# Performance work log

Hardware: AMD Instinct MI355X
Metric: run time of the kernel (lower is better)

The kernel has to match this reference:

```python
import jax, jax.numpy as jnp
import numpy as np
import math

N = 512      # sequence length (residues)
CS = 384     # single_embedding_size
CZ = 128     # pair_embedding_size
C = 16       # ipa_embedding_size
PQ = 4       # num_query_points
PV = 8       # num_value_points
H = 12       # num_heads

SCALE_SINGLE = 1.0 / math.sqrt(C)
SCALE_FRAME = -1.0 / math.sqrt(18 * PQ)


def setup_inputs() -> dict:
    key = jax.random.key(0)
    ks = jax.random.split(key, 14)
    w = lambda k, shape: jax.random.normal(k, shape, dtype=jnp.float32) * 0.02
    return {
        "single_rep": jax.random.normal(ks[0], (N, CS), dtype=jnp.float32),
        "pair_rep": jax.random.normal(ks[1], (N, N, CZ), dtype=jnp.float32),
        "rotations": jax.random.normal(ks[2], (N, 3, 3), dtype=jnp.float32),
        "translations": jax.random.normal(ks[3], (N, 3), dtype=jnp.float32),
        "Wq": w(ks[4], (CS, H * C)),
        "Wk": w(ks[5], (CS, H * C)),
        "Wv": w(ks[6], (CS, H * C)),
        "Wqp": w(ks[7], (CS, H * PQ * 3)),
        "Wkp": w(ks[8], (CS, H * PQ * 3)),
        "Wvp": w(ks[9], (CS, H * PV * 3)),
        "Wb": w(ks[10], (CZ, H)),
        "Wout": w(ks[11], (H * (CZ + C + PV * 4), CS)),
        "bout": jnp.zeros((CS,), dtype=jnp.float32),
        "scale_head": jnp.ones((H,), dtype=jnp.float32),
    }


def reference(single_rep, pair_rep, rotations, translations,
              Wq, Wk, Wv, Wqp, Wkp, Wvp, Wb, Wout, bout, scale_head):
    n = single_rep.shape[0]

    def apply_frames(x):  # x: [n, h, p, 3] -> R_n x + t_n
        return jnp.einsum('nij,nhpj->nhpi', rotations, x) + translations[:, None, None, :]

    # projections
    q = (single_rep @ Wq).reshape(n, H, C)
    k = (single_rep @ Wk).reshape(n, H, C)
    v = (single_rep @ Wv).reshape(n, H, C)
    qp = (single_rep @ Wqp).reshape(n, H, PQ, 3)
    kp = (single_rep @ Wkp).reshape(n, H, PQ, 3)
    vp = (single_rep @ Wvp).reshape(n, H, PV, 3)

    # single-rep weight: [n, H, n]
    w_single = SCALE_SINGLE * jnp.einsum('nhc,mhc->nhm', q, k)

    # pair-rep bias weight: [n, H, n]
    w_pair = jnp.einsum('nmz,zh->nhm', pair_rep, Wb)

    # frame (point) weight
    lq = apply_frames(qp)  # [n,H,PQ,3]
    lk = apply_frames(kp)  # [n,H,PQ,3]
    diff = lq[:, None] - lk[None, :]                 # [n,n,H,PQ,3]
    d2 = jnp.sum(diff * diff, axis=(-1, -2))         # [n,n,H]
    w_frame = SCALE_FRAME * jax.nn.softplus(scale_head)[None, :, None] \
              * jnp.transpose(d2, (0, 2, 1))         # [n,H,n]

    weight = jax.nn.softmax(w_single + w_pair + w_frame, axis=-1)  # [n,H,n]

    # attentions
    o_single = jnp.einsum('nhm,mhc->nhc', weight, v)            # [n,H,C]
    o_pair = jnp.einsum('nhm,nmz->nhz', weight, pair_rep)       # [n,H,CZ]

    lvp = apply_frames(vp)                                      # [n,H,PV,3]
    o_local = jnp.einsum('nhm,mhpc->nhpc', weight, lvp)         # [n,H,PV,3]
    # inverse frame: R^T (x - t)
    o_frame = jnp.einsum('nji,nhpj->nhpi', rotations,
                         o_local - translations[:, None, None, :])  # [n,H,PV,3]
    o_norm = jnp.linalg.norm(o_frame, axis=-1)                  # [n,H,PV]

    att = jnp.concatenate(
        [o_single, o_pair, o_frame.reshape(n, H, PV * 3), o_norm], axis=-1)
    return att.reshape(n, -1) @ Wout + bout
```

## Files before the change

kernel.cpp:

```cpp
#include <hip/hip_runtime.h>
#include <math.h>

#define NRES 512
#define CSZ  384
#define CZ   128
#define CC   16
#define PQ   4
#define PV   8
#define NH   12

#define HC    (NH*CC)
#define HPQ3  (NH*PQ*3)
#define HPV3  (NH*PV*3)
#define ATTD  (NH*(CZ+CC+PV*4))

#define OFF_Q   0
#define OFF_K   (OFF_Q  + NRES*HC)
#define OFF_V   (OFF_K  + NRES*HC)
#define OFF_LQ  (OFF_V  + NRES*HC)
#define OFF_LK  (OFF_LQ + NRES*HPQ3)
#define OFF_LVP (OFF_LK + NRES*HPQ3)
#define OFF_ATT (OFF_LVP+ NRES*HPV3)
#define OFF_LOG (OFF_ATT + NRES*ATTD)
#define OFF_PART OFF_LOG
#define LOG_FLOATS (NRES*NH*NRES)

#define OFF_KH  OFF_ATT
#define OFF_QH  (OFF_ATT + NH*NRES*32)

#define SCALE_SINGLE 0.25f
#define SCALE_FRAME  (-0.1178511301977579f)

#define LROW 516

#define PJ_BM 32
#define PJ_BN 64
#define PJ_BK 32
#define PJ_NK (CSZ/PJ_BK)
#define PJ_AP 388

__global__ __launch_bounds__(256) void k_proj2(
    const float* __restrict__ S,
    const float* __restrict__ Wq, const float* __restrict__ Wk,
    const float* __restrict__ Wv, const float* __restrict__ Wqp,
    const float* __restrict__ Wkp, const float* __restrict__ Wvp,
    float* __restrict__ ws)
{
  __shared__ __align__(16) float A_s[PJ_BM][PJ_AP];
  __shared__ __align__(16) float B_s[PJ_BK][PJ_BN];

  const int t  = threadIdx.x;
  const int rb = blockIdx.x / 18;
  const int cb = blockIdx.x % 18;
  const int tc = t & 15, tr = t >> 4;

  #pragma unroll
  for (int j = 0; j < 12; ++j) {
    int idx = t + j*256;
    int row = idx / 96, kq = idx % 96;
    float4 v4 = *(const float4*)(S + (size_t)(rb*PJ_BM + row)*CSZ + kq*4);
    *(float4*)&A_s[row][kq*4] = v4;
  }

  const float* Wp[2]; int ncB[2], lcB[2], kkB[2], cqB[2];
  #pragma unroll
  for (int j = 0; j < 2; ++j) {
    int idx = t + j*256;
    int kk = idx >> 4, cq = idx & 15;
    kkB[j] = kk; cqB[j] = cq;
    int col = cb*PJ_BN + cq*4;
    if      (col < 192) { Wp[j]=Wq;  ncB[j]=192; lcB[j]=col;     }
    else if (col < 384) { Wp[j]=Wk;  ncB[j]=192; lcB[j]=col-192; }
    else if (col < 576) { Wp[j]=Wv;  ncB[j]=192; lcB[j]=col-384; }
    else if (col < 720) { Wp[j]=Wqp; ncB[j]=144; lcB[j]=col-576; }
    else if (col < 864) { Wp[j]=Wkp; ncB[j]=144; lcB[j]=col-720; }
    else                { Wp[j]=Wvp; ncB[j]=288; lcB[j]=col-864; }
  }

  float4 bw[2];
  #pragma unroll
  for (int j = 0; j < 2; ++j)
    bw[j] = *(const float4*)(Wp[j] + (size_t)kkB[j]*ncB[j] + lcB[j]);

  float acc[2][4];
  #pragma unroll
  for (int i=0;i<2;i++)
    #pragma unroll
    for (int jj=0;jj<4;jj++) acc[i][jj]=0.f;

  for (int ki = 0; ki < PJ_NK; ++ki) {
    __syncthreads();
    #pragma unroll
    for (int j = 0; j < 2; ++j)
      *(float4*)&B_s[kkB[j]][cqB[j]*4] = bw[j];
    __syncthreads();

    if (ki + 1 < PJ_NK) {
      #pragma unroll
      for (int j = 0; j < 2; ++j)
        bw[j] = *(const float4*)(Wp[j] + (size_t)((ki+1)*PJ_BK + kkB[j])*ncB[j] + lcB[j]);
    }

    #pragma unroll
    for (int kk4 = 0; kk4 < PJ_BK/4; ++kk4) {
      float4 a0 = *(const float4*)&A_s[tr*2+0][ki*PJ_BK + kk4*4];
      float4 a1 = *(const float4*)&A_s[tr*2+1][ki*PJ_BK + kk4*4];
      const float* a0p = (const float*)&a0;
      const float* a1p = (const float*)&a1;
      #pragma unroll
      for (int e = 0; e < 4; ++e) {
        float4 b4 = *(const float4*)&B_s[kk4*4+e][tc*4];
        float f0 = a0p[e], f1 = a1p[e];
        acc[0][0] += f0*b4.x; acc[0][1] += f0*b4.y; acc[0][2] += f0*b4.z; acc[0][3] += f0*b4.w;
        acc[1][0] += f1*b4.x; acc[1][1] += f1*b4.y; acc[1][2] += f1*b4.z; acc[1][3] += f1*b4.w;
      }
    }
  }

  {
    int col = cb*PJ_BN + tc*4;
    float* dst; int stride; int lcc;
    if      (col < 192) { dst = ws+OFF_Q;   stride=192; lcc=col;     }
    else if (col < 384) { dst = ws+OFF_K;   stride=192; lcc=col-192; }
    else if (col < 576) { dst = ws+OFF_V;   stride=192; lcc=col-384; }
    else if (col < 720) { dst = ws+OFF_LQ;  stride=144; lcc=col-576; }
    else if (col < 864) { dst = ws+OFF_LK;  stride=144; lcc=col-720; }
    else                { dst = ws+OFF_LVP; stride=288; lcc=col-864; }
    #pragma unroll
    for (int i = 0; i < 2; ++i) {
      int row = rb*PJ_BM + tr*2 + i;
      *(float4*)&dst[(size_t)row*stride + lcc] =
          make_float4(acc[i][0], acc[i][1], acc[i][2], acc[i][3]);
    }
  }
}

__global__ __launch_bounds__(256) void k_frames(
    const float* __restrict__ rot, const float* __restrict__ trans,
    float* __restrict__ ws)
{
  int gid = blockIdx.x*256 + threadIdx.x;
  if (gid >= NRES*192) return;
  int m = gid / 192;
  int rest = gid % 192;
  float* base; int pidx;
  if      (rest <  48) { base = ws + OFF_LQ  + (size_t)m*HPQ3; pidx = rest;     }
  else if (rest <  96) { base = ws + OFF_LK  + (size_t)m*HPQ3; pidx = rest-48;  }
  else                 { base = ws + OFF_LVP + (size_t)m*HPV3; pidx = rest-96;  }
  float x = base[pidx*3+0], y = base[pidx*3+1], z = base[pidx*3+2];
  const float* R = rot + (size_t)m*9;
  const float* T = trans + (size_t)m*3;
  float o0 = R[0]*x + R[1]*y + R[2]*z + T[0];
  float o1 = R[3]*x + R[4]*y + R[5]*z + T[1];
  float o2 = R[6]*x + R[7]*y + R[8]*z + T[2];
  base[pidx*3+0]=o0; base[pidx*3+1]=o1; base[pidx*3+2]=o2;
}

__global__ __launch_bounds__(256) void k_hat(
    const float* __restrict__ scale_head, float* __restrict__ ws)
{
  const int r = blockIdx.x;
  const int t = threadIdx.x;
  __shared__ float sSp[NH];
  if (t < NH) { float x = scale_head[t];
                sSp[t] = (x > 20.f) ? x : log1pf(__expf(x)); }
  __syncthreads();

  for (int i = t; i < NH*32; i += 256) {
    const int h = i >> 5, j = i & 31;
    const float* kk = ws + OFF_K  + (size_t)r*HC   + h*CC;
    const float* lk = ws + OFF_LK + (size_t)r*HPQ3 + h*12;
    const float* qq = ws + OFF_Q  + (size_t)r*HC   + h*CC;
    const float* lq = ws + OFF_LQ + (size_t)r*HPQ3 + h*12;
    float kv, qv;
    if (j < 16)      { kv = kk[j];    qv = SCALE_SINGLE * qq[j]; }
    else if (j < 28) { kv = lk[j-16]; qv = -2.f*SCALE_FRAME*sSp[h]*lq[j-16]; }
    else if (j == 28) {
      float s2 = 0.f;
      #pragma unroll
      for (int e=0;e<12;e++) { float v = lk[e]; s2 += v*v; }
      kv = SCALE_FRAME * sSp[h] * s2;
      qv = 1.f;
    } else { kv = 0.f; qv = 0.f; }
    ws[OFF_KH + ((size_t)h*NRES + r)*32 + j] = kv;
    ws[OFF_QH + ((size_t)h*NRES + r)*32 + j] = qv;
  }
}

#define QK_P 68
__global__ __launch_bounds__(256) void k_qk(float* __restrict__ ws)
{
  __shared__ __align__(16) float Qs[32*QK_P];
  __shared__ __align__(16) float Ks[32*QK_P];

  const int bid = blockIdx.x;
  const int h  = bid >> 6;
  const int nt = (bid >> 3) & 7;
  const int mt = bid & 7;
  const int t  = threadIdx.x;
  const int tc = t & 15, tr = t >> 4;

  const float4* qsrc = (const float4*)(ws + OFF_QH + ((size_t)h*NRES + nt*64)*32);
  const float4* ksrc = (const float4*)(ws + OFF_KH + ((size_t)h*NRES + mt*64)*32);

  #pragma unroll
  for (int u = 0; u < 2; ++u) {
    int idx = t + u*256;
    int r = idx >> 3, j4 = idx & 7;
    float4 qv = qsrc[idx];
    float4 kv = ksrc[idx];
    Qs[(j4*4+0)*QK_P + r] = qv.x;
    Qs[(j4*4+1)*QK_P + r] = qv.y;
    Qs[(j4*4+2)*QK_P + r] = qv.z;
    Qs[(j4*4+3)*QK_P + r] = qv.w;
    Ks[(j4*4+0)*QK_P + r] = kv.x;
    Ks[(j4*4+1)*QK_P + r] = kv.y;
    Ks[(j4*4+2)*QK_P + r] = kv.z;
    Ks[(j4*4+3)*QK_P + r] = kv.w;
  }
  __syncthreads();

  float acc[4][4];
  #pragma unroll
  for (int i=0;i<4;i++)
    #pragma unroll
    for (int k2=0;k2<4;k2++) acc[i][k2]=0.f;

  #pragma unroll
  for (int j = 0; j < 32; ++j) {
    float4 qv = *(const float4*)&Qs[j*QK_P + tr*4];
    float4 kv = *(const float4*)&Ks[j*QK_P + tc*4];
    acc[0][0] += qv.x*kv.x; acc[0][1] += qv.x*kv.y; acc[0][2] += qv.x*kv.z; acc[0][3] += qv.x*kv.w;
    acc[1][0] += qv.y*kv.x; acc[1][1] += qv.y*kv.y; acc[1][2] += qv.y*kv.z; acc[1][3] += qv.y*kv.w;
    acc[2][0] += qv.z*kv.x; acc[2][1] += qv.z*kv.y; acc[2][2] += qv.z*kv.z; acc[2][3] += qv.z*kv.w;
    acc[3][0] += qv.w*kv.x; acc[3][1] += qv.w*kv.y; acc[3][2] += qv.w*kv.z; acc[3][3] += qv.w*kv.w;
  }

  float* wlog = ws + OFF_LOG;
  #pragma unroll
  for (int i = 0; i < 4; ++i) {
    int n = nt*64 + tr*4 + i;
    *(float4*)&wlog[((size_t)n*NH + h)*NRES + mt*64 + tc*4] =
        make_float4(acc[i][0], acc[i][1], acc[i][2], acc[i][3]);
  }
}

__global__ __launch_bounds__(512) void k_attn2(
    const float* __restrict__ pair,
    const float* __restrict__ rot, const float* __restrict__ trans,
    const float* __restrict__ Wb,
    float* __restrict__ ws)
{
  const int n = blockIdx.x;
  const int t = threadIdx.x;

  __shared__ __align__(16) float sLogit[NH*LROW];
  __shared__ __align__(16) float sOP[4][NH*CZ];
  __shared__ __align__(16) float sOL[HPV3];
  __shared__ float sR[9];
  __shared__ float sT[3];

  const float* v    = ws + OFF_V;
  const float* lvp  = ws + OFF_LVP;
  const float* wlog = ws + OFF_LOG;
  float* att = ws + OFF_ATT;

  if (t >= 488 && t < 497)      sR[t-488] = rot[(size_t)n*9 + (t-488)];
  else if (t >= 497 && t < 500) sT[t-497] = trans[(size_t)n*3 + (t-497)];
  __syncthreads();

  {
    const int m = t;
    float acch[NH];
    #pragma unroll
    for (int h=0;h<NH;h++) acch[h]=0.f;

    const float4* pr = (const float4*)(pair + ((size_t)n*NRES + m)*CZ);
    for (int zq = 0; zq < CZ/4; ++zq) {
      float4 p4 = pr[zq];
      const float* pp = (const float*)&p4;
      #pragma unroll
      for (int e=0;e<4;e++) {
        float pv_ = pp[e];
        const float* wrow = Wb + (size_t)(zq*4+e)*NH;
        #pragma unroll
        for (int h=0;h<NH;h++) acch[h] += pv_ * wrow[h];
      }
    }

    #pragma unroll
    for (int h=0;h<NH;h++) {
      acch[h] += wlog[((size_t)n*NH + h)*NRES + m];
      sLogit[h*LROW + m] = acch[h];
    }
  }
  __syncthreads();

  {
    int wave = t >> 6, lane = t & 63;
    for (int h = wave; h < NH; h += 8) {
      float x[8]; float mx = -1e30f;
      #pragma unroll
      for (int j=0;j<8;j++) { x[j] = sLogit[h*LROW + lane + j*64]; mx = fmaxf(mx, x[j]); }
      #pragma unroll
      for (int d=1; d<64; d<<=1) mx = fmaxf(mx, __shfl_xor(mx, d, 64));
      float s = 0.f;
      #pragma unroll
      for (int j=0;j<8;j++) { x[j] = __expf(x[j]-mx); s += x[j]; }
      #pragma unroll
      for (int d=1; d<64; d<<=1) s += __shfl_xor(s, d, 64);
      float inv = 1.f/s;
      #pragma unroll
      for (int j=0;j<8;j++) sLogit[h*LROW + lane + j*64] = x[j]*inv;
    }
  }
  __syncthreads();

  {
    const int zq = t & 31;
    const int hg = (t >> 5) & 3;
    const int mg = t >> 7;
    float a0[4] = {0,0,0,0}, a1[4] = {0,0,0,0}, a2[4] = {0,0,0,0};
    const float* pb = pair + (size_t)n*NRES*CZ + zq*4;
    for (int mb = 0; mb < 32; ++mb) {
      int m0 = mg*128 + mb*4;
      float4 w0 = *(const float4*)&sLogit[(hg+0)*LROW + m0];
      float4 w1 = *(const float4*)&sLogit[(hg+4)*LROW + m0];
      float4 w2 = *(const float4*)&sLogit[(hg+8)*LROW + m0];
      const float* w0p = (const float*)&w0;
      const float* w1p = (const float*)&w1;
      const float* w2p = (const float*)&w2;
      #pragma unroll
      for (int i=0;i<4;i++) {
        float4 p4 = *(const float4*)(pb + (size_t)(m0+i)*CZ);
        const float* pp = (const float*)&p4;
        float f0 = w0p[i], f1 = w1p[i], f2 = w2p[i];
        #pragma unroll
        for (int e=0;e<4;e++) {
          a0[e] += f0*pp[e]; a1[e] += f1*pp[e]; a2[e] += f2*pp[e];
        }
      }
    }
    *(float4*)&sOP[mg][(hg+0)*CZ + zq*4] = make_float4(a0[0],a0[1],a0[2],a0[3]);
    *(float4*)&sOP[mg][(hg+4)*CZ + zq*4] = make_float4(a1[0],a1[1],a1[2],a1[3]);
    *(float4*)&sOP[mg][(hg+8)*CZ + zq*4] = make_float4(a2[0],a2[1],a2[2],a2[3]);
  }

  {
    if (t < 480) {
      float acc = 0.f;
      const float* src; int stride; int off; int h;
      if (t < 192) { h = t >> 4;        src = v;   stride = HC;   off = t;      }
      else         { int idx = t - 192; h = idx/24; src = lvp; stride = HPV3; off = idx; }
      const float* wrow = sLogit + h*LROW;
      for (int m0 = 0; m0 < NRES; m0 += 4) {
        float4 w4 = *(const float4*)&wrow[m0];
        acc += w4.x * src[(size_t)(m0+0)*stride + off];
        acc += w4.y * src[(size_t)(m0+1)*stride + off];
        acc += w4.z * src[(size_t)(m0+2)*stride + off];
        acc += w4.w * src[(size_t)(m0+3)*stride + off];
      }
      if (t < 192) {
        int h2 = t >> 4;
        att[(size_t)n*ATTD + h2*176 + (t & 15)] = acc;
      } else {
        sOL[t-192] = acc;
      }
    }
  }
  __syncthreads();

  for (int o = t; o < NH*CZ; o += 512) {
    float sres = sOP[0][o] + sOP[1][o] + sOP[2][o] + sOP[3][o];
    int h = o >> 7, z = o & 127;
    att[(size_t)n*ATTD + h*176 + 16 + z] = sres;
  }

  if (t < 96) {
    int h = t / 8, p = t % 8;
    float x = sOL[h*24 + p*3 + 0] - sT[0];
    float y = sOL[h*24 + p*3 + 1] - sT[1];
    float z = sOL[h*24 + p*3 + 2] - sT[2];
    float o0 = sR[0]*x + sR[3]*y + sR[6]*z;
    float o1 = sR[1]*x + sR[4]*y + sR[7]*z;
    float o2 = sR[2]*x + sR[5]*y + sR[8]*z;
    float nm = sqrtf(o0*o0 + o1*o1 + o2*o2);
    float* ab = att + (size_t)n*ATTD + h*176;
    ab[144 + p*3 + 0] = o0;
    ab[144 + p*3 + 1] = o1;
    ab[144 + p*3 + 2] = o2;
    ab[168 + p] = nm;
  }
}

__global__ __launch_bounds__(512) void k_attn(
    const float* __restrict__ pair,
    const float* __restrict__ rot, const float* __restrict__ trans,
    const float* __restrict__ Wb, const float* __restrict__ scale_head,
    float* __restrict__ ws)
{
  const int n = blockIdx.x;
  const int t = threadIdx.x;

  __shared__ __align__(16) float sLogit[NH*LROW];
  __shared__ __align__(16) float sOP[4][NH*CZ];
  __shared__ __align__(16) float sQ[HC];
  __shared__ __align__(16) float sLQ[HPQ3];
  __shared__ float sSp[NH];
  __shared__ __align__(16) float sOL[HPV3];
  __shared__ float sR[9];
  __shared__ float sT[3];

  const float* q   = ws + OFF_Q;
  const float* k   = ws + OFF_K;
  const float* v   = ws + OFF_V;
  const float* lq  = ws + OFF_LQ;
  const float* lk  = ws + OFF_LK;
  const float* lvp = ws + OFF_LVP;
  float* att = ws + OFF_ATT;

  if (t < 192)               sQ[t]      = q[(size_t)n*HC + t];
  else if (t < 336)          sLQ[t-192] = lq[(size_t)n*HPQ3 + (t-192)];
  else if (t < 348) { float x = scale_head[t-336];
                      sSp[t-336] = (x > 20.f) ? x : log1pf(__expf(x)); }
  else if (t < 357)          sR[t-348]  = rot[(size_t)n*9 + (t-348)];
  else if (t < 360)          sT[t-357]  = trans[(size_t)n*3 + (t-357)];
  __syncthreads();

  {
    const int m = t;
    float acch[NH];
    #pragma unroll
    for (int h=0;h<NH;h++) acch[h]=0.f;

    const float4* pr = (const float4*)(pair + ((size_t)n*NRES + m)*CZ);
    for (int zq = 0; zq < CZ/4; ++zq) {
      float4 p4 = pr[zq];
      const float* pp = (const float*)&p4;
      #pragma unroll
      for (int e=0;e<4;e++) {
        float pv_ = pp[e];
        const float* wrow = Wb + (size_t)(zq*4+e)*NH;
        #pragma unroll
        for (int h=0;h<NH;h++) acch[h] += pv_ * wrow[h];
      }
    }

    #pragma unroll
    for (int h=0;h<NH;h++) {
      const float4* kr = (const float4*)(k + (size_t)m*HC + h*CC);
      const float* qrow = sQ + h*CC;
      float d = 0.f;
      #pragma unroll
      for (int j=0;j<4;j++) {
        float4 k4 = kr[j];
        d += k4.x*qrow[j*4+0] + k4.y*qrow[j*4+1] + k4.z*qrow[j*4+2] + k4.w*qrow[j*4+3];
      }
      acch[h] += SCALE_SINGLE * d;

      const float* lkr = lk + (size_t)m*HPQ3 + h*12;
      const float* lqr = sLQ + h*12;
      float d2 = 0.f;
      #pragma unroll
      for (int j=0;j<12;j++) { float df = lqr[j]-lkr[j]; d2 += df*df; }
      acch[h] += SCALE_FRAME * sSp[h] * d2;

      sLogit[h*LROW + m] = acch[h];
    }
  }
  __syncthreads();

  {
    int wave = t >> 6, lane = t & 63;
    for (int h = wave; h < NH; h += 8) {
      float x[8]; float mx = -1e30f;
      #pragma unroll
      for (int j=0;j<8;j++) { x[j] = sLogit[h*LROW + lane + j*64]; mx = fmaxf(mx, x[j]); }
      #pragma unroll
      for (int d=1; d<64; d<<=1) mx = fmaxf(mx, __shfl_xor(mx, d, 64));
      float s = 0.f;
      #pragma unroll
      for (int j=0;j<8;j++) { x[j] = __expf(x[j]-mx); s += x[j]; }
      #pragma unroll
      for (int d=1; d<64; d<<=1) s += __shfl_xor(s, d, 64);
      float inv = 1.f/s;
      #pragma unroll
      for (int j=0;j<8;j++) sLogit[h*LROW + lane + j*64] = x[j]*inv;
    }
  }
  __syncthreads();

  {
    const int zq = t & 31;
    const int hg = (t >> 5) & 3;
    const int mg = t >> 7;
    float a0[4] = {0,0,0,0}, a1[4] = {0,0,0,0}, a2[4] = {0,0,0,0};
    const float* pb = pair + (size_t)n*NRES*CZ + zq*4;
    for (int mb = 0; mb < 32; ++mb) {
      int m0 = mg*128 + mb*4;
      float4 w0 = *(const float4*)&sLogit[(hg+0)*LROW + m0];
      float4 w1 = *(const float4*)&sLogit[(hg+4)*LROW + m0];
      float4 w2 = *(const float4*)&sLogit[(hg+8)*LROW + m0];
      const float* w0p = (const float*)&w0;
      const float* w1p = (const float*)&w1;
      const float* w2p = (const float*)&w2;
      #pragma unroll
      for (int i=0;i<4;i++) {
        float4 p4 = *(const float4*)(pb + (size_t)(m0+i)*CZ);
        const float* pp = (const float*)&p4;
        float f0 = w0p[i], f1 = w1p[i], f2 = w2p[i];
        #pragma unroll
        for (int e=0;e<4;e++) {
          a0[e] += f0*pp[e]; a1[e] += f1*pp[e]; a2[e] += f2*pp[e];
        }
      }
    }
    *(float4*)&sOP[mg][(hg+0)*CZ + zq*4] = make_float4(a0[0],a0[1],a0[2],a0[3]);
    *(float4*)&sOP[mg][(hg+4)*CZ + zq*4] = make_float4(a1[0],a1[1],a1[2],a1[3]);
    *(float4*)&sOP[mg][(hg+8)*CZ + zq*4] = make_float4(a2[0],a2[1],a2[2],a2[3]);
  }

  {
    if (t < 480) {
      float acc = 0.f;
      const float* src; int stride; int off; int h;
      if (t < 192) { h = t >> 4;        src = v;   stride = HC;   off = t;      }
      else         { int idx = t - 192; h = idx/24; src = lvp; stride = HPV3; off = idx; }
      const float* wrow = sLogit + h*LROW;
      for (int m0 = 0; m0 < NRES; m0 += 4) {
        float4 w4 = *(const float4*)&wrow[m0];
        acc += w4.x * src[(size_t)(m0+0)*stride + off];
        acc += w4.y * src[(size_t)(m0+1)*stride + off];
        acc += w4.z * src[(size_t)(m0+2)*stride + off];
        acc += w4.w * src[(size_t)(m0+3)*stride + off];
      }
      if (t < 192) {
        int h2 = t >> 4;
        att[(size_t)n*ATTD + h2*176 + (t & 15)] = acc;
      } else {
        sOL[t-192] = acc;
      }
    }
  }
  __syncthreads();

  for (int o = t; o < NH*CZ; o += 512) {
    float sres = sOP[0][o] + sOP[1][o] + sOP[2][o] + sOP[3][o];
    int h = o >> 7, z = o & 127;
    att[(size_t)n*ATTD + h*176 + 16 + z] = sres;
  }

  if (t < 96) {
    int h = t / 8, p = t % 8;
    float x = sOL[h*24 + p*3 + 0] - sT[0];
    float y = sOL[h*24 + p*3 + 1] - sT[1];
    float z = sOL[h*24 + p*3 + 2] - sT[2];
    float o0 = sR[0]*x + sR[3]*y + sR[6]*z;
    float o1 = sR[1]*x + sR[4]*y + sR[7]*z;
    float o2 = sR[2]*x + sR[5]*y + sR[8]*z;
    float nm = sqrtf(o0*o0 + o1*o1 + o2*o2);
    float* ab = att + (size_t)n*ATTD + h*176;
    ab[144 + p*3 + 0] = o0;
    ab[144 + p*3 + 1] = o1;
    ab[144 + p*3 + 2] = o2;
    ab[168 + p] = nm;
  }
}

#define KOUT_BK 24

__global__ __launch_bounds__(256) void k_out_part(
    const float* __restrict__ ws, const float* __restrict__ Wout,
    float* __restrict__ part, int KS)
{
  const float* att = ws + OFF_ATT;
  const int bid  = blockIdx.x;
  const int ks   = bid / 48;
  const int tile = bid % 48;
  const int rb   = tile / 6, cb = tile % 6;
  const int KLEN = ATTD / KS;
  const int k0b  = ks * KLEN;

  __shared__ __align__(16) float A_s[64][KOUT_BK+1];
  __shared__ __align__(16) float B_s[KOUT_BK][64];

  const int t  = threadIdx.x;
  const int tc = t & 15, tr = t >> 4;

  float acc[4][4];
  #pragma unroll
  for (int i=0;i<4;i++)
    #pragma unroll
    for (int j=0;j<4;j++) acc[i][j]=0.f;

  for (int k0 = k0b; k0 < k0b + KLEN; k0 += KOUT_BK) {
    __syncthreads();
    #pragma unroll
    for (int j = 0; j < 6; ++j) {
      int idx = t + j*256;
      int r  = idx / KOUT_BK, kk = idx % KOUT_BK;
      A_s[r][kk] = att[(size_t)(rb*64 + r)*ATTD + k0 + kk];
      int kk2 = idx >> 6, c = idx & 63;
      B_s[kk2][c] = Wout[(size_t)(k0 + kk2)*CSZ + cb*64 + c];
    }
    __syncthreads();
    #pragma unroll
    for (int kk = 0; kk < KOUT_BK; ++kk) {
      float4 b4 = *(const float4*)&B_s[kk][tc*4];
      float a0 = A_s[tr*4+0][kk];
      float a1 = A_s[tr*4+1][kk];
      float a2 = A_s[tr*4+2][kk];
      float a3 = A_s[tr*4+3][kk];
      acc[0][0] += a0*b4.x; acc[0][1] += a0*b4.y; acc[0][2] += a0*b4.z; acc[0][3] += a0*b4.w;
      acc[1][0] += a1*b4.x; acc[1][1] += a1*b4.y; acc[1][2] += a1*b4.z; acc[1][3] += a1*b4.w;
      acc[2][0] += a2*b4.x; acc[2][1] += a2*b4.y; acc[2][2] += a2*b4.z; acc[2][3] += a2*b4.w;
      acc[3][0] += a3*b4.x; acc[3][1] += a3*b4.y; acc[3][2] += a3*b4.z; acc[3][3] += a3*b4.w;
    }
  }

  float* pb = part + (size_t)ks*NRES*CSZ;
  #pragma unroll
  for (int i=0;i<4;i++) {
    int row = rb*64 + tr*4 + i;
    int col = cb*64 + tc*4;
    *(float4*)&pb[(size_t)row*CSZ + col] =
        make_float4(acc[i][0], acc[i][1], acc[i][2], acc[i][3]);
  }
}

__global__ __launch_bounds__(256) void k_out_reduce(
    const float* __restrict__ part, const float* __restrict__ bout,
    float* __restrict__ out, int KS)
{
  int idx4 = blockIdx.x*256 + threadIdx.x;
  if (idx4 >= NRES*CSZ/4) return;
  int c4 = idx4 % (CSZ/4);
  float4 s = ((const float4*)bout)[c4];
  const float4* p4 = (const float4*)part;
  for (int ks = 0; ks < KS; ++ks) {
    float4 v = p4[(size_t)ks*(NRES*CSZ/4) + idx4];
    s.x += v.x; s.y += v.y; s.z += v.z; s.w += v.w;
  }
  ((float4*)out)[idx4] = s;
}

__global__ __launch_bounds__(256) void k_out_v1(
    const float* __restrict__ ws, const float* __restrict__ Wout,
    const float* __restrict__ bout, float* __restrict__ out)
{
  const float* att = ws + OFF_ATT;
  int cb = blockIdx.x % 6;
  int rb = blockIdx.x / 6;
  int t  = threadIdx.x;
  int c  = cb*64 + (t & 63);
  int rg = t >> 6;
  int r0 = rb*16;
  float acc[4] = {0.f,0.f,0.f,0.f};
  for (int a = 0; a < ATTD; ++a) {
    float wv = Wout[(size_t)a*CSZ + c];
    #pragma unroll
    for (int i=0;i<4;i++)
      acc[i] += att[(size_t)(r0 + rg + 4*i)*ATTD + a] * wv;
  }
  float b = bout[c];
  #pragma unroll
  for (int i=0;i<4;i++)
    out[(size_t)(r0 + rg + 4*i)*CSZ + c] = acc[i] + b;
}

extern "C" void kernel_launch(void* const* d_in, const int* in_sizes, int n_in,
                              void* d_out, int out_size, void* d_ws, size_t ws_size,
                              hipStream_t stream) {
  const float* S     = (const float*)d_in[0];
  const float* pair  = (const float*)d_in[1];
  const float* rot   = (const float*)d_in[2];
  const float* trans = (const float*)d_in[3];
  const float* Wq    = (const float*)d_in[4];
  const float* Wk    = (const float*)d_in[5];
  const float* Wv    = (const float*)d_in[6];
  const float* Wqp   = (const float*)d_in[7];
  const float* Wkp   = (const float*)d_in[8];
  const float* Wvp   = (const float*)d_in[9];
  const float* Wb    = (const float*)d_in[10];
  const float* Wout  = (const float*)d_in[11];
  const float* bout  = (const float*)d_in[12];
  const float* sh    = (const float*)d_in[13];
  float* out = (float*)d_out;
  float* ws  = (float*)d_ws;

  hipLaunchKernelGGL(k_proj2,  dim3(16*18), dim3(256), 0, stream,
                     S, Wq, Wk, Wv, Wqp, Wkp, Wvp, ws);
  hipLaunchKernelGGL(k_frames, dim3((NRES*192+255)/256), dim3(256), 0, stream,
                     rot, trans, ws);

  const size_t need_new = (size_t)(OFF_LOG + LOG_FLOATS) * sizeof(float);
  if (ws_size >= need_new) {
    hipLaunchKernelGGL(k_hat,   dim3(NRES), dim3(256), 0, stream, sh, ws);
    hipLaunchKernelGGL(k_qk,    dim3(NH*64), dim3(256), 0, stream, ws);
    hipLaunchKernelGGL(k_attn2, dim3(NRES), dim3(512), 0, stream,
                       pair, rot, trans, Wb, ws);
  } else {
    hipLaunchKernelGGL(k_attn,  dim3(NRES), dim3(512), 0, stream,
                       pair, rot, trans, Wb, sh, ws);
  }

  int KS = 0;
  const int cands[4] = {8, 4, 2, 1};
  for (int i = 0; i < 4; ++i) {
    size_t need = ((size_t)OFF_PART + (size_t)cands[i]*NRES*CSZ) * sizeof(float);
    if (need <= ws_size) { KS = cands[i]; break; }
  }
  if (KS > 0) {
    hipLaunchKernelGGL(k_out_part, dim3(48*KS), dim3(256), 0, stream,
                       ws, Wout, ws + OFF_PART, KS);
    hipLaunchKernelGGL(k_out_reduce, dim3((NRES*CSZ/4 + 255)/256), dim3(256), 0, stream,
                       ws + OFF_PART, bout, out, KS);
  } else {
    hipLaunchKernelGGL(k_out_v1, dim3(32*6), dim3(256), 0, stream,
                       ws, Wout, bout, out);
  }
}
```

Before: 168.7 us.

## Coalesce pair-bias loads with lane-split z and stage Wb in LDS

The pair-bias logits in k_attn2 are now computed with four lanes sharing each row. Each lane loads an interleaved float4 slice of z, so neighbouring lanes read contiguous memory instead of each thread streaming its own 512-byte row. Partial sums are reduced across the four lanes with xor shuffles, and each lane then writes three of the twelve heads. Wb is copied into shared memory and read as float4, replacing repeated scalar global reads, at the cost of 6 KB more LDS and 48 accumulator registers per thread.

Result: faster. 156.7 us (-7.1%).

```diff
diff --git a/kernel.cpp b/kernel.cpp
--- a/kernel.cpp
+++ b/kernel.cpp
@@ -256,6 +256,7 @@
 
   __shared__ __align__(16) float sLogit[NH*LROW];
   __shared__ __align__(16) float sOP[4][NH*CZ];
+  __shared__ __align__(16) float sWb[CZ*NH];
   __shared__ __align__(16) float sOL[HPV3];
   __shared__ float sR[9];
   __shared__ float sT[3];
@@ -267,31 +268,74 @@
 
   if (t >= 488 && t < 497)      sR[t-488] = rot[(size_t)n*9 + (t-488)];
   else if (t >= 497 && t < 500) sT[t-497] = trans[(size_t)n*3 + (t-497)];
-  __syncthreads();
-
-  {
-    const int m = t;
-    float acch[NH];
-    #pragma unroll
-    for (int h=0;h<NH;h++) acch[h]=0.f;
-
-    const float4* pr = (const float4*)(pair + ((size_t)n*NRES + m)*CZ);
-    for (int zq = 0; zq < CZ/4; ++zq) {
-      float4 p4 = pr[zq];
-      const float* pp = (const float*)&p4;
-      #pragma unroll
-      for (int e=0;e<4;e++) {
-        float pv_ = pp[e];
-        const float* wrow = Wb + (size_t)(zq*4+e)*NH;
-        #pragma unroll
-        for (int h=0;h<NH;h++) acch[h] += pv_ * wrow[h];
-      }
-    }
-
-    #pragma unroll
-    for (int h=0;h<NH;h++) {
-      acch[h] += wlog[((size_t)n*NH + h)*NRES + m];
-      sLogit[h*LROW + m] = acch[h];
+  for (int i = t; i < CZ*NH; i += 512) sWb[i] = Wb[i];
+  __syncthreads();
+
+  {
+    const int q  = t & 3;
+    const int r0 = t >> 2;
+    float accb[4][12];
+    #pragma unroll
+    for (int j=0;j<4;++j)
+      #pragma unroll
+      for (int h=0;h<12;++h) accb[j][h] = 0.f;
+
+    const float4* pr4 = (const float4*)(pair + (size_t)n*NRES*CZ);
+
+    #pragma unroll 1
+    for (int zc = 0; zc < 8; ++zc) {
+      float4 p0 = pr4[(size_t)(r0 +   0)*32 + zc*4 + q];
+      float4 p1 = pr4[(size_t)(r0 + 128)*32 + zc*4 + q];
+      float4 p2 = pr4[(size_t)(r0 + 256)*32 + zc*4 + q];
+      float4 p3 = pr4[(size_t)(r0 + 384)*32 + zc*4 + q];
+      #pragma unroll
+      for (int e = 0; e < 4; ++e) {
+        const float* wz = &sWb[(size_t)(zc*16 + q*4 + e)*12];
+        float4 w0 = *(const float4*)&wz[0];
+        float4 w1 = *(const float4*)&wz[4];
+        float4 w2 = *(const float4*)&wz[8];
+#define ACC_J(J, PV)                                                  \
+        { float f = ((const float*)&PV)[e];                           \
+          accb[J][0]  += f*w0.x; accb[J][1]  += f*w0.y;               \
+          accb[J][2]  += f*w0.z; accb[J][3]  += f*w0.w;               \
+          accb[J][4]  += f*w1.x; accb[J][5]  += f*w1.y;               \
+          accb[J][6]  += f*w1.z; accb[J][7]  += f*w1.w;               \
+          accb[J][8]  += f*w2.x; accb[J][9]  += f*w2.y;               \
+          accb[J][10] += f*w2.z; accb[J][11] += f*w2.w; }
+        ACC_J(0, p0) ACC_J(1, p1) ACC_J(2, p2) ACC_J(3, p3)
+#undef ACC_J
+      }
+    }
+
+    #pragma unroll
+    for (int j=0;j<4;++j)
+      #pragma unroll
+      for (int h=0;h<12;++h) {
+        accb[j][h] += __shfl_xor(accb[j][h], 1, 64);
+        accb[j][h] += __shfl_xor(accb[j][h], 2, 64);
+      }
+
+    float sel[3][4];
+    #pragma unroll
+    for (int i = 0; i < 3; ++i)
+      #pragma unroll
+      for (int j = 0; j < 4; ++j) {
+        float vv = accb[j][i];
+        vv = (q == 1) ? accb[j][3+i] : vv;
+        vv = (q == 2) ? accb[j][6+i] : vv;
+        vv = (q == 3) ? accb[j][9+i] : vv;
+        sel[i][j] = vv;
+      }
+
+    #pragma unroll
+    for (int i = 0; i < 3; ++i) {
+      const int h = q*3 + i;
+      const size_t base = ((size_t)n*NH + h)*NRES;
+      #pragma unroll
+      for (int j = 0; j < 4; ++j) {
+        const int row = r0 + j*128;
+        sLogit[h*LROW + row] = sel[i][j] + wlog[base + row];
+      }
     }
   }
   __syncthreads();
```
